# Kernel tuning notes

Measured on AMD Instinct MI355X. Metric: run time of the kernel, lower is better.

Reference implementation:

```python
import jax, jax.numpy as jnp
import numpy as np
import math

EMB, QK, V, HEAD = 512, 64, 64, 8
B, S = 8, 2048

def setup_inputs() -> dict:
    key = jax.random.key(0)
    ks = jax.random.split(key, 10)
    sc = 1.0 / math.sqrt(EMB)
    return {
        "x_q": jax.random.normal(ks[0], (B, S, EMB), jnp.float32),
        "x_k_v": jax.random.normal(ks[1], (B, S, EMB), jnp.float32),
        "attn_mask": jax.random.randint(ks[2], (B, S, S), 0, 2, jnp.int32),
        "w_q": jax.random.normal(ks[3], (HEAD * QK, EMB), jnp.float32) * sc,
        "b_q": jax.random.normal(ks[4], (HEAD * QK,), jnp.float32) * sc,
        "w_k": jax.random.normal(ks[5], (HEAD * QK, EMB), jnp.float32) * sc,
        "b_k": jax.random.normal(ks[6], (HEAD * QK,), jnp.float32) * sc,
        "w_v": jax.random.normal(ks[7], (HEAD * V, EMB), jnp.float32) * sc,
        "b_v": jax.random.normal(ks[8], (HEAD * V,), jnp.float32) * sc,
    }

def reference(x_q, x_k_v, attn_mask, w_q, b_q, w_k, b_k, w_v, b_v):
    Bq, Sq, _ = x_q.shape
    Skv = x_k_v.shape[1]
    # linear projections (torch Linear: x @ W.T + b)
    q = (x_q @ w_q.T + b_q).reshape(Bq, Sq, HEAD, QK)     # [B,Sq,H,Dk]
    k = (x_k_v @ w_k.T + b_k).reshape(Bq, Skv, HEAD, QK)  # [B,Skv,H,Dk]
    v = (x_k_v @ w_v.T + b_v).reshape(Bq, Skv, HEAD, V)   # [B,Skv,H,Dv]
    # scores [B,H,Sq,Skv]
    attn = jnp.einsum("bqhd,bkhd->bhqk", q, k) / math.sqrt(QK)
    mask = attn_mask[:, None, :, :].astype(bool)
    attn = jnp.where(mask, jnp.float32(-1e9), attn)
    attn = jax.nn.softmax(attn, axis=-1)
    z = jnp.einsum("bhqk,bkhd->bqhd", attn, v)            # [B,Sq,H,Dv]
    return z.reshape(Bq, Sq, HEAD * V)
```

## Files before the change

kernel.cpp:

```cpp
#include <hip/hip_runtime.h>
#include <hip/hip_bf16.h>
#include <math.h>

typedef float  f32x4  __attribute__((ext_vector_type(4)));
typedef float  f32x16 __attribute__((ext_vector_type(16)));
typedef short  s16x8  __attribute__((ext_vector_type(8)));
typedef __bf16 bf16x8 __attribute__((ext_vector_type(8)));
typedef unsigned int u32;
typedef unsigned int u32x4 __attribute__((ext_vector_type(4)));
typedef unsigned short u16;
typedef unsigned long long u64;

#define DEVI static __device__ __forceinline__

#if defined(__has_builtin) && __has_builtin(__builtin_amdgcn_exp2f)
#define EXP2(x) __builtin_amdgcn_exp2f(x)
#else
#define EXP2(x) exp2f(x)
#endif

DEVI u32 cvtpk(float lo, float hi) {
  u32 r;
  asm("v_cvt_pk_bf16_f32 %0, %1, %2" : "=v"(r) : "v"(lo), "v"(hi));
  return r;
}

DEVI f32x4 mfma_bf16(s16x8 a, s16x8 b, f32x4 c) {
  return __builtin_amdgcn_mfma_f32_16x16x32_bf16(
      __builtin_bit_cast(bf16x8, a), __builtin_bit_cast(bf16x8, b), c, 0, 0, 0);
}

DEVI f32x16 mfma32(s16x8 a, s16x8 b, f32x16 c) {
  return __builtin_amdgcn_mfma_f32_32x32x16_bf16(
      __builtin_bit_cast(bf16x8, a), __builtin_bit_cast(bf16x8, b), c, 0, 0, 0);
}

DEVI void gload_lds16(const void* g, void* l) {
  __builtin_amdgcn_global_load_lds(
      (const __attribute__((address_space(1))) void*)g,
      (__attribute__((address_space(3))) void*)l, 16, 0, 0);
}

__global__ __launch_bounds__(256)
void mask_pack(const int* __restrict__ mask, u64* __restrict__ mp) {
  const int t = threadIdx.x, lane = t & 63;
  const int gw = blockIdx.x * 4 + (t >> 6);
  const int kt = gw & 31, q = (gw >> 5) & 2047, b = gw >> 16;
  int mv = mask[((size_t)b * 2048 + q) * 2048 + kt * 64 + lane];
  u64 bits = __ballot(mv == 0);
  if (lane == 0) mp[((size_t)b * 32 + kt) * 2048 + q] = bits;
}

__global__ __launch_bounds__(256, 2)
void qkv_proj(const float* __restrict__ xq, const float* __restrict__ xkv,
              const float* __restrict__ wq, const float* __restrict__ bq,
              const float* __restrict__ wk, const float* __restrict__ bk,
              const float* __restrict__ wv, const float* __restrict__ bv,
              u16* __restrict__ Qo, u16* __restrict__ Ko, u16* __restrict__ VTo)
{
  __shared__ __align__(16) char smem[128 * 272];
  char* lds_a = smem;
  char* lds_b = smem + 8192;

  const int t = threadIdx.x, lane = t & 63, w = t >> 6;
  const int z = blockIdx.z;
  const float* X  = (z == 0) ? xq : xkv;
  const float* W  = (z == 0) ? wq : (z == 1 ? wk : wv);
  const float* Bv = (z == 0) ? bq : (z == 1 ? bk : bv);

  const int m0 = blockIdx.x * 128, n0 = blockIdx.y * 128;
  const int wr = w >> 1, wc = w & 1, g = lane >> 4, q15 = lane & 15;
  const int srow = t >> 1, shalf = t & 1;

  f32x4 acc[4][4];
  #pragma unroll
  for (int i = 0; i < 4; ++i)
    #pragma unroll
    for (int j = 0; j < 4; ++j) acc[i][j] = (f32x4){0.f, 0.f, 0.f, 0.f};

  const float* gA = X + (size_t)(m0 + srow) * 512 + shalf * 16;
  const float* gB = W + (size_t)(n0 + srow) * 512 + shalf * 16;
  const int wbyte = srow * 64;
  const int sw = (srow & 3) << 4;

  #pragma unroll 1
  for (int kt = 0; kt < 16; ++kt) {
    float4 fa[4], fb[4];
    #pragma unroll
    for (int j = 0; j < 4; ++j) {
      fa[j] = *(const float4*)(gA + kt * 32 + j * 4);
      fb[j] = *(const float4*)(gB + kt * 32 + j * 4);
    }
    __syncthreads();
    const float* pfa = (const float*)fa;
    const float* pfb = (const float*)fb;
    #pragma unroll
    for (int half = 0; half < 2; ++half) {
      u32x4 wa, wb;
      #pragma unroll
      for (int e2 = 0; e2 < 4; ++e2) {
        wa[e2] = cvtpk(pfa[half * 8 + 2 * e2], pfa[half * 8 + 2 * e2 + 1]);
        wb[e2] = cvtpk(pfb[half * 8 + 2 * e2], pfb[half * 8 + 2 * e2 + 1]);
      }
      *(u32x4*)(lds_a + wbyte + ((shalf * 32 + half * 16) ^ sw)) = wa;
      *(u32x4*)(lds_b + wbyte + ((shalf * 32 + half * 16) ^ sw)) = wb;
    }
    __syncthreads();
    s16x8 afr[4], bfr[4];
    #pragma unroll
    for (int mi = 0; mi < 4; ++mi) {
      int row = wr * 64 + mi * 16 + q15;
      afr[mi] = *(const s16x8*)(lds_a + row * 64 + ((g * 16) ^ ((row & 3) << 4)));
    }
    #pragma unroll
    for (int ni = 0; ni < 4; ++ni) {
      int row = wc * 64 + ni * 16 + q15;
      bfr[ni] = *(const s16x8*)(lds_b + row * 64 + ((g * 16) ^ ((row & 3) << 4)));
    }
    #pragma unroll
    for (int mi = 0; mi < 4; ++mi)
      #pragma unroll
      for (int ni = 0; ni < 4; ++ni)
        acc[mi][ni] = mfma_bf16(afr[mi], bfr[ni], acc[mi][ni]);
  }

  float bias[4];
  #pragma unroll
  for (int ni = 0; ni < 4; ++ni) bias[ni] = Bv[n0 + wc * 64 + ni * 16 + q15];

  if (z < 2) {
    u16* Out = z ? Ko : Qo;
    const float scale = z ? 1.0f : 0.18033688011112042f;
    #pragma unroll
    for (int mi = 0; mi < 4; ++mi)
      #pragma unroll
      for (int ni = 0; ni < 4; ++ni)
        #pragma unroll
        for (int r = 0; r < 4; r += 2) {
          int m = m0 + wr * 64 + mi * 16 + g * 4 + r;
          int n = n0 + wc * 64 + ni * 16 + q15;
          u32 pk = cvtpk((acc[mi][ni][r] + bias[ni]) * scale,
                         (acc[mi][ni][r + 1] + bias[ni]) * scale);
          Out[(size_t)m * 512 + n]       = (u16)pk;
          Out[(size_t)(m + 1) * 512 + n] = (u16)(pk >> 16);
        }
  } else {
    __syncthreads();
    #pragma unroll
    for (int mi = 0; mi < 4; ++mi)
      #pragma unroll
      for (int ni = 0; ni < 4; ++ni)
        #pragma unroll
        for (int r = 0; r < 4; r += 2) {
          int ml = wr * 64 + mi * 16 + g * 4 + r;
          int nl = wc * 64 + ni * 16 + q15;
          *(u32*)(smem + nl * 272 + ml * 2) =
              cvtpk(acc[mi][ni][r] + bias[ni], acc[mi][ni][r + 1] + bias[ni]);
        }
    __syncthreads();
    const int b  = m0 >> 11;
    const int s0 = m0 & 2047;
    #pragma unroll
    for (int nn = 0; nn < 2; ++nn) {
      int n  = nn * 64 + (t >> 2);
      int q4 = t & 3;
      u16* dst = VTo + (size_t)(b * 512 + n0 + n) * 2048 + s0 + q4 * 32;
      #pragma unroll
      for (int jj = 0; jj < 4; ++jj)
        *(s16x8*)(dst + jj * 8) = *(const s16x8*)(smem + n * 272 + q4 * 64 + jj * 16);
    }
  }
}

__global__ __launch_bounds__(256, 3)
void attn_fwd(const u16* __restrict__ Q, const u16* __restrict__ K,
              const u16* __restrict__ VT, const u64* __restrict__ MP,
              float* __restrict__ out)
{
  __shared__ __align__(16) char lds_k[2][8192];
  __shared__ __align__(16) char lds_v[2][8192];

  const int bid = blockIdx.x;
  const int h = bid & 7, b = (bid >> 3) & 7, qt = bid >> 6;
  const int t = threadIdx.x, lane = t & 63, w = t >> 6;
  const int l31 = lane & 31, hi = lane >> 5;
  const int qbase = qt * 128 + w * 32;
  const int swz = (l31 & 7) << 4;

  s16x8 qf[4];
  #pragma unroll
  for (int j = 0; j < 4; ++j)
    qf[j] = *(const s16x8*)(Q + (size_t)(b * 2048 + qbase + l31) * 512
                              + h * 64 + j * 16 + hi * 8);
  asm volatile("" ::: "memory");

  f32x16 o0 = {0.f,0.f,0.f,0.f,0.f,0.f,0.f,0.f,0.f,0.f,0.f,0.f,0.f,0.f,0.f,0.f};
  f32x16 o1 = o0, o2 = o0;
  const f32x16 ZZ = o0;
  const s16x8 onesf = {0x3F80,0x3F80,0x3F80,0x3F80,0x3F80,0x3F80,0x3F80,0x3F80};

  const int srow8 = lane >> 3, slot = lane & 7;
  const int rl0 = w * 16 + srow8, rl1 = rl0 + 8;

  const u16* kP0 = K + (size_t)(b * 2048 + rl0) * 512 + h * 64 + (slot ^ (rl0 & 7)) * 8;
  const u16* kP1 = K + (size_t)(b * 2048 + rl1) * 512 + h * 64 + (slot ^ (rl1 & 7)) * 8;
  const u16* vP0 = VT + (size_t)(b * 512 + h * 64 + rl0) * 2048 + (slot ^ (rl0 & 7)) * 8;
  const u16* vP1 = VT + (size_t)(b * 512 + h * 64 + rl1) * 2048 + (slot ^ (rl1 & 7)) * 8;
  const u64* mpP = MP + (size_t)b * 32 * 2048 + qbase + l31;

  gload_lds16(kP0, &lds_k[0][w * 2048]);
  gload_lds16(vP0, &lds_v[0][w * 2048]);
  gload_lds16(kP1, &lds_k[0][w * 2048 + 1024]);
  gload_lds16(vP1, &lds_v[0][w * 2048 + 1024]);
  asm volatile("" ::: "memory");
  u64 pm = *mpP;

  #pragma unroll 1
  for (int kt = 0; kt < 32; ++kt) {
    const int cur = kt & 1;
    const u64 kw = pm;
    if (kt + 1 < 32) {
      kP0 += 32768; kP1 += 32768; vP0 += 64; vP1 += 64; mpP += 2048;
      gload_lds16(kP0, &lds_k[cur ^ 1][w * 2048]);
      gload_lds16(vP0, &lds_v[cur ^ 1][w * 2048]);
      gload_lds16(kP1, &lds_k[cur ^ 1][w * 2048 + 1024]);
      gload_lds16(vP1, &lds_v[cur ^ 1][w * 2048 + 1024]);
      asm volatile("" ::: "memory");
      pm = *mpP;
      asm volatile("s_waitcnt vmcnt(5)" ::: "memory");
    } else {
      asm volatile("s_waitcnt vmcnt(0)" ::: "memory");
    }
    asm volatile("s_barrier" ::: "memory");

    f32x16 p0, p1;
    {
      s16x8 a0 = *(const s16x8*)(&lds_k[cur][ l31       * 128 + ((0 * 32 + hi * 16) ^ swz)]);
      s16x8 a1 = *(const s16x8*)(&lds_k[cur][(l31 + 32) * 128 + ((0 * 32 + hi * 16) ^ swz)]);
      p0 = mfma32(a0, qf[0], ZZ);
      p1 = mfma32(a1, qf[0], ZZ);
    }
    #pragma unroll
    for (int j = 1; j < 4; ++j) {
      s16x8 a0 = *(const s16x8*)(&lds_k[cur][ l31       * 128 + ((j * 32 + hi * 16) ^ swz)]);
      s16x8 a1 = *(const s16x8*)(&lds_k[cur][(l31 + 32) * 128 + ((j * 32 + hi * 16) ^ swz)]);
      p0 = mfma32(a0, qf[j], p0);
      p1 = mfma32(a1, qf[j], p1);
    }

    u64 kws = kw >> (hi * 4);
    u32 mm0 = (u32)kws, mm1 = (u32)(kws >> 32);
    u32 wds[16];
    #pragma unroll
    for (int t2 = 0; t2 < 2; ++t2) {
      const u32 mmw = t2 ? mm1 : mm0;
      #pragma unroll
      for (int q = 0; q < 8; ++q) {
        const int bp = 8 * (q >> 1) + 2 * (q & 1);
        float s0v = t2 ? p1[2 * q] : p0[2 * q];
        float s1v = t2 ? p1[2 * q + 1] : p0[2 * q + 1];
        float e0 = EXP2(s0v), e1 = EXP2(s1v);
        u32 k0 = (u32)((int)(mmw << (31 - bp)) >> 31);
        u32 k1 = (u32)((int)(mmw << (30 - bp)) >> 31);
        e0 = __builtin_bit_cast(float, __builtin_bit_cast(u32, e0) & k0);
        e1 = __builtin_bit_cast(float, __builtin_bit_cast(u32, e1) & k1);
        wds[t2 * 8 + q] = cvtpk(e0, e1);
      }
    }

    #pragma unroll
    for (int j = 0; j < 4; ++j) {
      const int ia = 2 * j, ib = 2 * j + 1;
      u32 wa0 = wds[(ia >> 2) * 8 + 2 * (ia & 3)];
      u32 wa1 = wds[(ia >> 2) * 8 + 2 * (ia & 3) + 1];
      u32 wb0 = wds[(ib >> 2) * 8 + 2 * (ib & 3)];
      u32 wb1 = wds[(ib >> 2) * 8 + 2 * (ib & 3) + 1];
      asm("v_permlane32_swap_b32 %0, %1" : "+v"(wa0), "+v"(wb0));
      asm("v_permlane32_swap_b32 %0, %1" : "+v"(wa1), "+v"(wb1));
      u32x4 aw = {wa0, wa1, wb0, wb1};
      s16x8 af = __builtin_bit_cast(s16x8, aw);
      s16x8 v0 = *(const s16x8*)(&lds_v[cur][ l31       * 128 + ((j * 32 + hi * 16) ^ swz)]);
      s16x8 v1 = *(const s16x8*)(&lds_v[cur][(l31 + 32) * 128 + ((j * 32 + hi * 16) ^ swz)]);
      o0 = mfma32(af, v0, o0);
      o1 = mfma32(af, v1, o1);
      o2 = mfma32(af, onesf, o2);
    }

    asm volatile("s_waitcnt lgkmcnt(0)" ::: "memory");
    __builtin_amdgcn_sched_barrier(0);
    asm volatile("s_barrier" ::: "memory");
  }

  #pragma unroll
  for (int reg = 0; reg < 16; ++reg) {
    const int ql = (reg & 3) + 8 * (reg >> 2) + 4 * hi;
    const float linv = 1.0f / o2[reg];
    float* po = out + (size_t)(b * 2048 + qbase + ql) * 512 + h * 64 + l31;
    po[0]  = o0[reg] * linv;
    po[32] = o1[reg] * linv;
  }
}

extern "C" void kernel_launch(void* const* d_in, const int* in_sizes, int n_in,
                              void* d_out, int out_size, void* d_ws, size_t ws_size,
                              hipStream_t stream) {
  const float* xq  = (const float*)d_in[0];
  const float* xkv = (const float*)d_in[1];
  const int*   msk = (const int*)d_in[2];
  const float* wq  = (const float*)d_in[3];
  const float* bq  = (const float*)d_in[4];
  const float* wk  = (const float*)d_in[5];
  const float* bk  = (const float*)d_in[6];
  const float* wv  = (const float*)d_in[7];
  const float* bv  = (const float*)d_in[8];

  u16* Qw = (u16*)d_ws;
  u16* Kw = Qw + (size_t)16384 * 512;
  u16* VT = Kw + (size_t)16384 * 512;
  u64* MP = (u64*)(VT + (size_t)4096 * 2048);

  mask_pack<<<dim3(131072), 256, 0, stream>>>(msk, MP);
  qkv_proj<<<dim3(128, 4, 3), 256, 0, stream>>>(xq, xkv, wq, bq, wk, bk, wv, bv,
                                                Qw, Kw, VT);
  attn_fwd<<<dim3(1024), 256, 0, stream>>>(Qw, Kw, VT, MP, (float*)d_out);
}
```

Before: 229.4 us.

## Batch mask packing per wave, restructure attention loop barriers and priorities

mask_pack now has each wave process 16 mask rows with a two-deep software prefetch, so the grid is 16x smaller and the mask reads are coalesced into contiguous packed-word writes. In attn_fwd the per-iteration synchronisation moves to the top of the loop as a single full wait plus barrier, replacing the split vmcnt(5) wait and trailing barrier. MFMA sections are wrapped in s_setprio so waves doing matrix work get issue priority. Launch bounds drop from 3 to 2 blocks per SIMD, which gives more registers per thread but lowers occupancy. The full vmcnt(0) wait at the loop head may expose the latency of the next tile's prefetch.

Result: faster. 219.0 us (-4.5%).

```diff
diff --git a/kernel.cpp b/kernel.cpp
--- a/kernel.cpp
+++ b/kernel.cpp
@@ -44,11 +44,20 @@
 __global__ __launch_bounds__(256)
 void mask_pack(const int* __restrict__ mask, u64* __restrict__ mp) {
   const int t = threadIdx.x, lane = t & 63;
-  const int gw = blockIdx.x * 4 + (t >> 6);
-  const int kt = gw & 31, q = (gw >> 5) & 2047, b = gw >> 16;
-  int mv = mask[((size_t)b * 2048 + q) * 2048 + kt * 64 + lane];
-  u64 bits = __ballot(mv == 0);
-  if (lane == 0) mp[((size_t)b * 32 + kt) * 2048 + q] = bits;
+  const u32 gw = blockIdx.x * 4 + (t >> 6);
+  const u32 W0 = gw * 16;
+  #define MSRC(W) ((((size_t)((W) >> 16) * 2048 + ((W) & 2047u)) * 2048) \
+                   + (((W) >> 11) & 31u) * 64 + lane)
+  int c0 = mask[MSRC(W0)];
+  int c1 = mask[MSRC(W0 + 1)];
+  #pragma unroll 4
+  for (u32 k = 0; k < 16; ++k) {
+    u64 bits = __ballot(c0 == 0);
+    if (lane == 0) mp[W0 + k] = bits;
+    c0 = c1;
+    if (k + 2 < 16) c1 = mask[MSRC(W0 + k + 2)];
+  }
+  #undef MSRC
 }
 
 __global__ __launch_bounds__(256, 2)
@@ -172,7 +181,7 @@
   }
 }
 
-__global__ __launch_bounds__(256, 3)
+__global__ __launch_bounds__(256, 2)
 void attn_fwd(const u16* __restrict__ Q, const u16* __restrict__ K,
               const u16* __restrict__ VT, const u64* __restrict__ MP,
               float* __restrict__ out)
@@ -219,6 +228,9 @@
   for (int kt = 0; kt < 32; ++kt) {
     const int cur = kt & 1;
     const u64 kw = pm;
+    asm volatile("s_waitcnt vmcnt(0) lgkmcnt(0)" ::: "memory");
+    __builtin_amdgcn_sched_barrier(0);
+    asm volatile("s_barrier" ::: "memory");
     if (kt + 1 < 32) {
       kP0 += 32768; kP1 += 32768; vP0 += 64; vP1 += 64; mpP += 2048;
       gload_lds16(kP0, &lds_k[cur ^ 1][w * 2048]);
@@ -226,27 +238,19 @@
       gload_lds16(kP1, &lds_k[cur ^ 1][w * 2048 + 1024]);
       gload_lds16(vP1, &lds_v[cur ^ 1][w * 2048 + 1024]);
       asm volatile("" ::: "memory");
-      pm = *mpP;
-      asm volatile("s_waitcnt vmcnt(5)" ::: "memory");
-    } else {
-      asm volatile("s_waitcnt vmcnt(0)" ::: "memory");
-    }
-    asm volatile("s_barrier" ::: "memory");
-
-    f32x16 p0, p1;
-    {
-      s16x8 a0 = *(const s16x8*)(&lds_k[cur][ l31       * 128 + ((0 * 32 + hi * 16) ^ swz)]);
-      s16x8 a1 = *(const s16x8*)(&lds_k[cur][(l31 + 32) * 128 + ((0 * 32 + hi * 16) ^ swz)]);
-      p0 = mfma32(a0, qf[0], ZZ);
-      p1 = mfma32(a1, qf[0], ZZ);
-    }
-    #pragma unroll
-    for (int j = 1; j < 4; ++j) {
+      pm = mpP[0];
+    }
+
+    f32x16 p0 = ZZ, p1 = ZZ;
+    __builtin_amdgcn_s_setprio(1);
+    #pragma unroll
+    for (int j = 0; j < 4; ++j) {
       s16x8 a0 = *(const s16x8*)(&lds_k[cur][ l31       * 128 + ((j * 32 + hi * 16) ^ swz)]);
       s16x8 a1 = *(const s16x8*)(&lds_k[cur][(l31 + 32) * 128 + ((j * 32 + hi * 16) ^ swz)]);
       p0 = mfma32(a0, qf[j], p0);
       p1 = mfma32(a1, qf[j], p1);
     }
+    __builtin_amdgcn_s_setprio(0);
 
     u64 kws = kw >> (hi * 4);
     u32 mm0 = (u32)kws, mm1 = (u32)(kws >> 32);
@@ -255,19 +259,20 @@
     for (int t2 = 0; t2 < 2; ++t2) {
       const u32 mmw = t2 ? mm1 : mm0;
       #pragma unroll
-      for (int q = 0; q < 8; ++q) {
-        const int bp = 8 * (q >> 1) + 2 * (q & 1);
-        float s0v = t2 ? p1[2 * q] : p0[2 * q];
-        float s1v = t2 ? p1[2 * q + 1] : p0[2 * q + 1];
+      for (int q2 = 0; q2 < 8; ++q2) {
+        const int bp = 8 * (q2 >> 1) + 2 * (q2 & 1);
+        float s0v = t2 ? p1[2 * q2] : p0[2 * q2];
+        float s1v = t2 ? p1[2 * q2 + 1] : p0[2 * q2 + 1];
         float e0 = EXP2(s0v), e1 = EXP2(s1v);
         u32 k0 = (u32)((int)(mmw << (31 - bp)) >> 31);
         u32 k1 = (u32)((int)(mmw << (30 - bp)) >> 31);
         e0 = __builtin_bit_cast(float, __builtin_bit_cast(u32, e0) & k0);
         e1 = __builtin_bit_cast(float, __builtin_bit_cast(u32, e1) & k1);
-        wds[t2 * 8 + q] = cvtpk(e0, e1);
+        wds[t2 * 8 + q2] = cvtpk(e0, e1);
       }
     }
 
+    __builtin_amdgcn_s_setprio(1);
     #pragma unroll
     for (int j = 0; j < 4; ++j) {
       const int ia = 2 * j, ib = 2 * j + 1;
@@ -285,10 +290,7 @@
       o1 = mfma32(af, v1, o1);
       o2 = mfma32(af, onesf, o2);
     }
-
-    asm volatile("s_waitcnt lgkmcnt(0)" ::: "memory");
-    __builtin_amdgcn_sched_barrier(0);
-    asm volatile("s_barrier" ::: "memory");
+    __builtin_amdgcn_s_setprio(0);
   }
 
   #pragma unroll
@@ -319,7 +321,7 @@
   u16* VT = Kw + (size_t)16384 * 512;
   u64* MP = (u64*)(VT + (size_t)4096 * 2048);
 
-  mask_pack<<<dim3(131072), 256, 0, stream>>>(msk, MP);
+  mask_pack<<<dim3(8192), 256, 0, stream>>>(msk, MP);
   qkv_proj<<<dim3(128, 4, 3), 256, 0, stream>>>(xq, xkv, wq, bq, wk, bk, wv, bv,
                                                 Qw, Kw, VT);
   attn_fwd<<<dim3(1024), 256, 0, stream>>>(Qw, Kw, VT, MP, (float*)d_out);
```
